# Kernel tuning notes

Measured on AMD Instinct MI355X. Metric: run time of the kernel, lower is better.

Reference implementation:

```python
import jax, jax.numpy as jnp
import numpy as np

D = 1024      # input_size / d_model
H = 16        # num_heads
HD = D // H   # head_size = 64
T = 2048      # block_size / seq_len
B = 2
FF = 4 * D
EPS = 1e-5


def setup_inputs() -> dict:
    key = jax.random.key(0)
    ks = jax.random.split(key, 16)
    s_in = 1.0 / np.sqrt(D)
    s_ff = 1.0 / np.sqrt(FF)
    return {
        "x": jax.random.normal(ks[0], (B, T, D), dtype=jnp.float32),
        # per-head unbiased projections, stacked over heads: [H, D, HD]
        "wq": jax.random.normal(ks[1], (H, D, HD), dtype=jnp.float32) * s_in,
        "wk": jax.random.normal(ks[2], (H, D, HD), dtype=jnp.float32) * s_in,
        "wv": jax.random.normal(ks[3], (H, D, HD), dtype=jnp.float32) * s_in,
        "w_proj": jax.random.normal(ks[4], (D, D), dtype=jnp.float32) * s_in,
        "b_proj": jnp.zeros((D,), dtype=jnp.float32),
        "ln1_g": jnp.ones((D,), dtype=jnp.float32),
        "ln1_b": jnp.zeros((D,), dtype=jnp.float32),
        "ln2_g": jnp.ones((D,), dtype=jnp.float32),
        "ln2_b": jnp.zeros((D,), dtype=jnp.float32),
        "w1": jax.random.normal(ks[5], (D, FF), dtype=jnp.float32) * s_in,
        "b1": jnp.zeros((FF,), dtype=jnp.float32),
        "w2": jax.random.normal(ks[6], (FF, D), dtype=jnp.float32) * s_ff,
        "b2": jnp.zeros((D,), dtype=jnp.float32),
    }


def _layernorm(x, g, b):
    mu = jnp.mean(x, axis=-1, keepdims=True)
    var = jnp.mean(jnp.square(x - mu), axis=-1, keepdims=True)
    return (x - mu) * jax.lax.rsqrt(var + EPS) * g + b


def reference(x, wq, wk, wv, w_proj, b_proj, ln1_g, ln1_b, ln2_g, ln2_b, w1, b1, w2, b2):
    Bv, Tv, _ = x.shape
    h = _layernorm(x, ln1_g, ln1_b)                       # [B,T,D]
    q = jnp.einsum("btc,hcd->bhtd", h, wq)
    k = jnp.einsum("btc,hcd->bhtd", h, wk)
    v = jnp.einsum("btc,hcd->bhtd", h, wv)
    scores = jnp.einsum("bhtd,bhsd->bhts", q, k) * (HD ** -0.5)  # [B,H,T,T]
    causal = jnp.tril(jnp.ones((Tv, Tv), dtype=bool))
    scores = jnp.where(causal, scores, -jnp.inf)
    attn = jax.nn.softmax(scores, axis=-1)
    out = jnp.einsum("bhts,bhsd->bhtd", attn, v)          # [B,H,T,HD]
    out = out.transpose(0, 2, 1, 3).reshape(Bv, Tv, H * HD)  # concat heads
    out = out @ w_proj + b_proj
    x = x + out
    h2 = _layernorm(x, ln2_g, ln2_b)
    ff = jax.nn.gelu(h2 @ w1 + b1, approximate=False) @ w2 + b2
    return x + ff
```

## Files before the change

### kernel.cpp

```cpp
#include <hip/hip_runtime.h>
#include <hip/hip_bf16.h>
#include <cstdint>
#include <cstddef>
#include <math.h>

#define D_ 1024
#define H_ 16
#define HD_ 64
#define T_ 2048
#define B_ 2
#define FF_ 4096
#define BT_ (B_*T_)
#define NT_ 32

typedef unsigned short u16;
typedef __attribute__((ext_vector_type(8))) __bf16 bf16x8;
typedef __attribute__((ext_vector_type(8))) u16 u16x8;
typedef __attribute__((ext_vector_type(4))) float f32x4;

__device__ __forceinline__ u16 f2bf(float f) {
  unsigned u = __builtin_bit_cast(unsigned, f);
  u += 0x7FFFu + ((u >> 16) & 1u);
  return (u16)(u >> 16);
}

__device__ __forceinline__ unsigned cvt_pk_bf16(float a, float b) {
  unsigned r;
  asm("v_cvt_pk_bf16_f32 %0, %1, %2" : "=v"(r) : "v"(a), "v"(b));
  return r;
}

__device__ __forceinline__ void gload16(const void* g, void* l) {
  __builtin_amdgcn_global_load_lds((__attribute__((address_space(1))) void*)g,
                                   (__attribute__((address_space(3))) void*)l, 16, 0, 0);
}

__global__ __launch_bounds__(256) void transpose_all(
    const float* __restrict__ wq, const float* __restrict__ wk,
    const float* __restrict__ wv, const float* __restrict__ w_proj,
    const float* __restrict__ w1, const float* __restrict__ w2,
    u16* __restrict__ wqkv_t, u16* __restrict__ wproj_t,
    u16* __restrict__ w1t, u16* __restrict__ w2t) {
  __shared__ float tile[32][33];
  const int bid = blockIdx.x;
  const float* in; u16* out; int R, C, tx, ty;
  if (bid < 3072) {
    const int w = bid >> 10, rem = bid & 1023;
    const int z = rem >> 6, t = rem & 63;
    tx = t & 1; ty = t >> 1;
    R = D_; C = HD_;
    in  = (w == 0 ? wq : w == 1 ? wk : wv) + (size_t)z * R * C;
    out = wqkv_t + (size_t)w * D_ * D_ + (size_t)z * C * R;
  } else if (bid < 4096) {
    const int t = bid - 3072;
    tx = t & 31; ty = t >> 5;
    R = D_; C = D_; in = w_proj; out = wproj_t;
  } else if (bid < 8192) {
    const int t = bid - 4096;
    tx = t & 127; ty = t >> 7;
    R = D_; C = FF_; in = w1; out = w1t;
  } else {
    const int t = bid - 8192;
    tx = t & 31; ty = t >> 5;
    R = FF_; C = D_; in = w2; out = w2t;
  }
  const int x = tx * 32 + threadIdx.x;
  const int y0 = ty * 32 + threadIdx.y;
  #pragma unroll
  for (int j = 0; j < 32; j += 8)
    tile[threadIdx.y + j][threadIdx.x] = in[(size_t)(y0 + j) * C + x];
  __syncthreads();
  const int orr = ty * 32 + threadIdx.x;
  const int oc0 = tx * 32 + threadIdx.y;
  #pragma unroll
  for (int j = 0; j < 32; j += 8)
    out[(size_t)(oc0 + j) * R + orr] = f2bf(tile[threadIdx.x][threadIdx.y + j]);
}

__global__ __launch_bounds__(256) void ln_rows(const float* __restrict__ x,
    const float* __restrict__ g, const float* __restrict__ bb, u16* __restrict__ out) {
  const int row = blockIdx.x, tid = threadIdx.x;
  const float4 v = ((const float4*)(x + (size_t)row * D_))[tid];
  float s = v.x + v.y + v.z + v.w;
  float sq = v.x*v.x + v.y*v.y + v.z*v.z + v.w*v.w;
  #pragma unroll
  for (int m = 1; m < 64; m <<= 1) { s += __shfl_xor(s, m); sq += __shfl_xor(sq, m); }
  __shared__ float ss[4], qs[4];
  if ((tid & 63) == 0) { ss[tid >> 6] = s; qs[tid >> 6] = sq; }
  __syncthreads();
  s  = ss[0] + ss[1] + ss[2] + ss[3];
  sq = qs[0] + qs[1] + qs[2] + qs[3];
  const float mean = s * (1.f / D_);
  const float var  = sq * (1.f / D_) - mean * mean;
  const float rstd = rsqrtf(var + 1e-5f);
  const float4 gv = ((const float4*)g)[tid];
  const float4 bv = ((const float4*)bb)[tid];
  u16 o[4];
  o[0] = f2bf((v.x - mean) * rstd * gv.x + bv.x);
  o[1] = f2bf((v.y - mean) * rstd * gv.y + bv.y);
  o[2] = f2bf((v.z - mean) * rstd * gv.z + bv.z);
  o[3] = f2bf((v.w - mean) * rstd * gv.w + bv.w);
  *(ushort4*)(out + (size_t)row * D_ + tid * 4) = *(ushort4*)o;
}

template<int ACT, int BIAS, int OUTBF, int PARTIAL>
__global__ __launch_bounds__(256, 4) void gemm128(
    const u16* __restrict__ A, const u16* __restrict__ Bt,
    const float* __restrict__ bias, const float* resid,
    void* Cout, int M, int N, int K, int Kper) {
  __shared__ __attribute__((aligned(16))) u16 LA[2][128 * 32];
  __shared__ __attribute__((aligned(16))) u16 LB[2][128 * 32];

  const int tid = threadIdx.x;
  const int wid = tid >> 6, lane = tid & 63;
  const int wr = wid >> 1, wc = wid & 1;
  const int frow = lane & 15, hi = lane >> 4;

  const int gx = gridDim.x;
  const int nwg = gx * gridDim.y;
  const int orig = blockIdx.y * gx + blockIdx.x;
  const int cpx = nwg >> 3;
  const int swz = (orig & 7) * cpx + (orig >> 3);
  const int bm = (swz / gx) * 128, bn = (swz % gx) * 128;
  const int z = PARTIAL ? blockIdx.z : 0;
  const int koff = z * Kper;
  const int nt = Kper >> 5;

  const int srow = tid >> 2;
  const int gch  = (tid & 3) ^ (srow & 3);
  const u16* Ag0 = A + (size_t)(bm + srow) * K + koff + gch * 8;
  const u16* Ag1 = Ag0 + (size_t)64 * K;
  const u16* Bg0 = Bt + (size_t)(bn + srow) * K + koff + gch * 8;
  const u16* Bg1 = Bg0 + (size_t)64 * K;
  const int ldsA0 = (wid * 16) * 32, ldsA1 = (64 + wid * 16) * 32;

  f32x4 acc[4][4] = {};

  #define STAGE32(kt, db)                              \
    {                                                  \
      const int ko = (kt) * 32;                        \
      gload16(Ag0 + ko, &LA[db][ldsA0]);               \
      gload16(Ag1 + ko, &LA[db][ldsA1]);               \
      gload16(Bg0 + ko, &LB[db][ldsA0]);               \
      gload16(Bg1 + ko, &LB[db][ldsA1]);               \
    }

  STAGE32(0, 0);

  for (int t = 0; t < nt; ++t) {
    const int db = t & 1;
    if (t + 1 < nt) {
      STAGE32(t + 1, db ^ 1);
      asm volatile("s_waitcnt vmcnt(4)" ::: "memory");
    } else {
      asm volatile("s_waitcnt vmcnt(0)" ::: "memory");
    }
    __builtin_amdgcn_s_barrier();

    const u16* Ab = &LA[db][0];
    const u16* Bb = &LB[db][0];

    bf16x8 af[4], bfr[4];
    #pragma unroll
    for (int i = 0; i < 4; i++) {
      const int ra = wr * 64 + i * 16 + frow;
      af[i]  = *(const bf16x8*)(Ab + ra * 32 + ((hi ^ (ra & 3)) << 3));
      const int rb = wc * 64 + i * 16 + frow;
      bfr[i] = *(const bf16x8*)(Bb + rb * 32 + ((hi ^ (rb & 3)) << 3));
    }
    __builtin_amdgcn_s_setprio(1);
    #pragma unroll
    for (int mi = 0; mi < 4; mi++)
      #pragma unroll
      for (int ni = 0; ni < 4; ni++)
        acc[mi][ni] = __builtin_amdgcn_mfma_f32_16x16x32_bf16(af[mi], bfr[ni], acc[mi][ni], 0, 0, 0);
    __builtin_amdgcn_s_setprio(0);
    __builtin_amdgcn_s_barrier();
  }
  #undef STAGE32

  const int r0 = bm + wr * 64 + hi * 4;
  const int c0 = bn + wc * 64 + frow;
  #pragma unroll
  for (int mi = 0; mi < 4; mi++) {
    #pragma unroll
    for (int ni = 0; ni < 4; ni++) {
      #pragma unroll
      for (int r = 0; r < 4; r++) {
        float v = acc[mi][ni][r];
        const int rr = r0 + mi * 16 + r;
        const int cc = c0 + ni * 16;
        if (PARTIAL) {
          ((float*)Cout)[((size_t)z * M + rr) * N + cc] = v;
        } else {
          if (BIAS) v += bias[cc];
          if (ACT == 1) {
            const float u = v * (0.79788456f + 0.03567740814f * v * v);
            const float e = exp2f(fminf(u * 2.885390082f, 80.f));
            v = v - v * __builtin_amdgcn_rcpf(1.0f + e);
          }
          if (resid) v += resid[(size_t)rr * N + cc];
          if (OUTBF) ((u16*)Cout)[(size_t)rr * N + cc] = f2bf(v);
          else       ((float*)Cout)[(size_t)rr * N + cc] = v;
        }
      }
    }
  }
}

template<int NPART>
__global__ __launch_bounds__(256) void reduce_parts(
    const float* __restrict__ parts, const float* __restrict__ bias,
    const float* __restrict__ resid, float* __restrict__ out, int MN, int N) {
  const int i4 = (blockIdx.x * 256 + threadIdx.x) * 4;
  if (i4 >= MN) return;
  float4 s = *(const float4*)(parts + i4);
  #pragma unroll
  for (int p = 1; p < NPART; p++) {
    const float4 t = *(const float4*)(parts + (size_t)p * MN + i4);
    s.x += t.x; s.y += t.y; s.z += t.z; s.w += t.w;
  }
  const float4 bv = *(const float4*)(bias + (i4 & (N - 1)));
  const float4 rv = *(const float4*)(resid + i4);
  s.x += bv.x + rv.x; s.y += bv.y + rv.y; s.z += bv.z + rv.z; s.w += bv.w + rv.w;
  *(float4*)(out + i4) = s;
}

__global__ __launch_bounds__(256) void reduce2_ln(
    const float* __restrict__ parts, const float* __restrict__ bias,
    const float* __restrict__ resid, const float* __restrict__ g,
    const float* __restrict__ bb, float* __restrict__ xout,
    u16* __restrict__ h2, int MN) {
  const int row = blockIdx.x, tid = threadIdx.x;
  const int i4 = row * D_ + tid * 4;
  float4 s = *(const float4*)(parts + i4);
  const float4 t = *(const float4*)(parts + (size_t)MN + i4);
  const float4 bv = *(const float4*)(bias + tid * 4);
  const float4 rv = *(const float4*)(resid + i4);
  s.x += t.x + bv.x + rv.x; s.y += t.y + bv.y + rv.y;
  s.z += t.z + bv.z + rv.z; s.w += t.w + bv.w + rv.w;
  *(float4*)(xout + i4) = s;
  float sm = s.x + s.y + s.z + s.w;
  float sq = s.x*s.x + s.y*s.y + s.z*s.z + s.w*s.w;
  #pragma unroll
  for (int m = 1; m < 64; m <<= 1) { sm += __shfl_xor(sm, m); sq += __shfl_xor(sq, m); }
  __shared__ float ss[4], qs[4];
  if ((tid & 63) == 0) { ss[tid >> 6] = sm; qs[tid >> 6] = sq; }
  __syncthreads();
  sm = ss[0] + ss[1] + ss[2] + ss[3];
  sq = qs[0] + qs[1] + qs[2] + qs[3];
  const float mean = sm * (1.f / D_);
  const float var  = sq * (1.f / D_) - mean * mean;
  const float rstd = rsqrtf(var + 1e-5f);
  const float4 gv = ((const float4*)g)[tid];
  const float4 b2v = ((const float4*)bb)[tid];
  u16 o[4];
  o[0] = f2bf((s.x - mean) * rstd * gv.x + b2v.x);
  o[1] = f2bf((s.y - mean) * rstd * gv.y + b2v.y);
  o[2] = f2bf((s.z - mean) * rstd * gv.z + b2v.z);
  o[3] = f2bf((s.w - mean) * rstd * gv.w + b2v.w);
  *(ushort4*)(h2 + (size_t)row * D_ + tid * 4) = *(ushort4*)o;
}

__global__ __launch_bounds__(256) void repack_qkv(const u16* __restrict__ qkv,
    u16* __restrict__ q, u16* __restrict__ k, u16* __restrict__ vt) {
  const int t0 = blockIdx.x * 64, bh = blockIdx.y;
  const int b = bh >> 4, h = bh & 15;
  const int tid = threadIdx.x;
  const int c = (tid & 7) * 8;
  __shared__ __attribute__((aligned(16))) u16 vs[64][72];
  #pragma unroll
  for (int p = 0; p < 2; p++) {
    const int tl = p * 32 + (tid >> 3);
    const size_t inrow = ((size_t)b * T_ + t0 + tl) * 3072 + h * 64;
    u16x8 qv = *(const u16x8*)(qkv + inrow + c);
    bf16x8 kv = *(const bf16x8*)(qkv + inrow + 1024 + c);
    bf16x8 vv = *(const bf16x8*)(qkv + inrow + 2048 + c);
    alignas(16) u16 qs[8];
    #pragma unroll
    for (int e = 0; e < 8; e++) {
      const float f = __builtin_bit_cast(float, ((unsigned)qv[e]) << 16) * 0.18033688011112042f;
      qs[e] = f2bf(f);
    }
    *(u16x8*)(q + ((size_t)bh * T_ + t0 + tl) * HD_ + c) = *(u16x8*)qs;
    *(bf16x8*)(k + ((size_t)bh * T_ + t0 + tl) * HD_ + c) = kv;
    *(bf16x8*)&vs[tl][c] = vv;
  }
  __syncthreads();
  const int d = tid >> 2, tc = (tid & 3) * 16;
  alignas(16) u16 tmp[16];
  #pragma unroll
  for (int j = 0; j < 16; j++) tmp[j] = vs[tc + j][d];
  *(bf16x8*)(vt + ((size_t)bh * HD_ + d) * T_ + t0 + tc)     = *(bf16x8*)&tmp[0];
  *(bf16x8*)(vt + ((size_t)bh * HD_ + d) * T_ + t0 + tc + 8) = *(bf16x8*)&tmp[8];
}

__global__ __launch_bounds__(512) void attn_fwd(
    const u16* __restrict__ q, const u16* __restrict__ k,
    const u16* __restrict__ vt, u16* __restrict__ out) {
  __shared__ __attribute__((aligned(16))) u16 Ps[8][16 * 64];
  __shared__ __attribute__((aligned(16))) u16 Kb[2][64 * 64];
  __shared__ __attribute__((aligned(16))) u16 Vb[2][64 * 64];

  const int bid = blockIdx.x;
  const int xcd = bid & 7, j = bid >> 3;
  const int bh  = xcd + 8 * (j & 3);
  const int qb  = 15 - (j >> 2);
  const int b = bh >> 4, h = bh & 15;
  const int tid = threadIdx.x, wid = tid >> 6, lane = tid & 63;
  const u16* kh = k  + (size_t)bh * T_ * HD_;
  const u16* vh = vt + (size_t)bh * HD_ * T_;
  const int q0 = qb * 128;
  const int nkt = 2 * qb + 2;
  const int wlast = 2 * qb + (wid >> 2);

  const int frow = lane & 15;
  const int hi   = lane >> 4;
  const int fk   = hi * 8;
  const int rowb = hi * 4;
  const int colb = frow;
  const int srow = tid >> 3;
  const int gch  = (tid & 7) ^ (srow & 7);

  u16x8 onebits = (u16x8)((u16)0x3F80);
  bf16x8 b_one = (frow == 0) ? __builtin_bit_cast(bf16x8, onebits) : (bf16x8){};

  u16* Pw = &Ps[wid][0];

  const u16* qrow = q + ((size_t)bh * T_ + q0 + wid * 16 + frow) * HD_;
  bf16x8 aq[2];
  aq[0] = *(const bf16x8*)(qrow + fk);
  aq[1] = *(const bf16x8*)(qrow + 32 + fk);

  float m2[4] = {-3e38f, -3e38f, -3e38f, -3e38f};
  f32x4 acc_l = {};
  f32x4 acc_o[4] = {};

  int cur = 0;
  gload16(kh + (size_t)srow * HD_ + gch * 8, &Kb[0][(wid * 8) * 64]);
  gload16(vh + (size_t)srow * T_ + gch * 8,  &Vb[0][(wid * 8) * 64]);
  __syncthreads();

  for (int kt = 0; kt < nkt; ++kt) {
    if (kt + 1 < nkt) {
      const int nx = cur ^ 1, ktn = kt + 1;
      gload16(kh + (size_t)(ktn * 64 + srow) * HD_ + gch * 8, &Kb[nx][(wid * 8) * 64]);
      gload16(vh + (size_t)srow * T_ + ktn * 64 + gch * 8,    &Vb[nx][(wid * 8) * 64]);
    }

    if (kt <= wlast) {
      const u16* Kc = &Kb[cur][0];
      const u16* Vc = &Vb[cur][0];

      float p2[4][4];
      __builtin_amdgcn_s_setprio(1);
      #pragma unroll
      for (int ni = 0; ni < 4; ni++) {
        f32x4 s = {};
        #pragma unroll
        for (int ks = 0; ks < 2; ks++) {
          const int row = ni * 16 + frow;
          const int ch  = ks * 4 + hi;
          bf16x8 bk = *(const bf16x8*)(Kc + row * 64 + ((ch ^ (row & 7)) << 3));
          s = __builtin_amdgcn_mfma_f32_16x16x32_bf16(aq[ks], bk, s, 0, 0, 0);
        }
        #pragma unroll
        for (int r = 0; r < 4; r++) p2[ni][r] = s[r];
      }
      __builtin_amdgcn_s_setprio(0);

      if (kt >= nkt - 2) {
        #pragma unroll
        for (int ni = 0; ni < 4; ni++)
          #pragma unroll
          for (int r = 0; r < 4; r++) {
            const bool msk = (kt * 64 + ni * 16 + colb) > (q0 + wid * 16 + rowb + r);
            if (msk) p2[ni][r] = -3e38f;
          }
      }

      float lmax[4];
      #pragma unroll
      for (int r = 0; r < 4; r++)
        lmax[r] = fmaxf(fmaxf(p2[0][r], p2[1][r]), fmaxf(p2[2][r], p2[3][r]));
      int ok = 1;
      #pragma unroll
      for (int r = 0; r < 4; r++) ok &= (lmax[r] <= m2[r] + 8.0f);
      if (!__all(ok)) {
        #pragma unroll
        for (int r = 0; r < 4; r++) {
          float rm = lmax[r];
          rm = fmaxf(rm, __shfl_xor(rm, 1));
          rm = fmaxf(rm, __shfl_xor(rm, 2));
          rm = fmaxf(rm, __shfl_xor(rm, 4));
          rm = fmaxf(rm, __shfl_xor(rm, 8));
          const float mnew = fmaxf(m2[r], rm);
          const float corr = exp2f(m2[r] - mnew);
          m2[r] = mnew;
          acc_l[r] *= corr;
          #pragma unroll
          for (int ni = 0; ni < 4; ni++) acc_o[ni][r] *= corr;
        }
      }
      #pragma unroll
      for (int ni = 0; ni < 4; ni++)
        #pragma unroll
        for (int r = 0; r < 4; r++) p2[ni][r] = exp2f(p2[ni][r] - m2[r]);

      #pragma unroll
      for (int ni = 0; ni < 4; ni++) {
        #pragma unroll
        for (int r = 0; r < 4; r += 2) {
          const unsigned pk = cvt_pk_bf16(p2[ni][r], p2[ni][r + 1]);
          const int lr0 = rowb + r, lr1 = rowb + r + 1;
          const int ch = ni * 2 + (colb >> 3);
          Pw[lr0 * 64 + ((ch ^ (lr0 & 7)) << 3) + (colb & 7)] = (u16)pk;
          Pw[lr1 * 64 + ((ch ^ (lr1 & 7)) << 3) + (colb & 7)] = (u16)(pk >> 16);
        }
      }
      bf16x8 ap[2];
      {
        const int c0 = (0 * 4 + hi) ^ (frow & 7);
        const int c1 = (1 * 4 + hi) ^ (frow & 7);
        ap[0] = *(const bf16x8*)(Pw + frow * 64 + (c0 << 3));
        ap[1] = *(const bf16x8*)(Pw + frow * 64 + (c1 << 3));
      }

      __builtin_amdgcn_s_setprio(1);
      #pragma unroll
      for (int ks = 0; ks < 2; ks++)
        acc_l = __builtin_amdgcn_mfma_f32_16x16x32_bf16(ap[ks], b_one, acc_l, 0, 0, 0);
      #pragma unroll
      for (int ni = 0; ni < 4; ni++) {
        #pragma unroll
        for (int ks = 0; ks < 2; ks++) {
          const int row = ni * 16 + frow;
          const int ch  = ks * 4 + hi;
          bf16x8 bv = *(const bf16x8*)(Vc + row * 64 + ((ch ^ (row & 7)) << 3));
          acc_o[ni] = __builtin_amdgcn_mfma_f32_16x16x32_bf16(ap[ks], bv, acc_o[ni], 0, 0, 0);
        }
      }
      __builtin_amdgcn_s_setprio(0);
    }

    __syncthreads();
    cur ^= 1;
  }

  float linv[4];
  #pragma unroll
  for (int r = 0; r < 4; r++) {
    const float lv = __shfl(acc_l[r], lane & 48);
    linv[r] = 1.0f / lv;
  }
  #pragma unroll
  for (int ni = 0; ni < 4; ni++)
    #pragma unroll
    for (int r = 0; r < 4; r++) {
      const float ov = acc_o[ni][r] * linv[r];
      const size_t row = (size_t)b * T_ + q0 + wid * 16 + rowb + r;
      out[row * D_ + h * HD_ + ni * 16 + colb] = f2bf(ov);
    }
}

extern "C" void kernel_launch(void* const* d_in, const int* in_sizes, int n_in,
                              void* d_out, int out_size, void* d_ws, size_t ws_size,
                              hipStream_t stream) {
  (void)in_sizes; (void)n_in; (void)out_size; (void)ws_size;
  const float* x      = (const float*)d_in[0];
  const float* wq     = (const float*)d_in[1];
  const float* wk     = (const float*)d_in[2];
  const float* wv     = (const float*)d_in[3];
  const float* w_proj = (const float*)d_in[4];
  const float* b_proj = (const float*)d_in[5];
  const float* ln1_g  = (const float*)d_in[6];
  const float* ln1_b  = (const float*)d_in[7];
  const float* ln2_g  = (const float*)d_in[8];
  const float* ln2_b  = (const float*)d_in[9];
  const float* w1     = (const float*)d_in[10];
  const float* b1     = (const float*)d_in[11];
  const float* w2     = (const float*)d_in[12];
  const float* b2     = (const float*)d_in[13];

  uint8_t* ws = (uint8_t*)d_ws;
  const size_t MB = 1024 * 1024;
  u16* wqkv_t = (u16*)(ws + 0);
  u16* wproj_t = (u16*)(ws + 6 * MB);
  u16* w1t  = (u16*)(ws + 8 * MB);
  u16* w2t  = (u16*)(ws + 16 * MB);
  u16* hbuf = (u16*)(ws + 24 * MB);
  u16* qkv  = (u16*)(ws + 32 * MB);
  u16* qb   = (u16*)(ws + 56 * MB);
  u16* kb   = (u16*)(ws + 64 * MB);
  u16* vtb  = (u16*)(ws + 72 * MB);
  u16* aout = (u16*)(ws + 80 * MB);
  u16* h2   = (u16*)(ws + 88 * MB);
  u16* ff1  = (u16*)(ws + 96 * MB);
  float* pparts = (float*)(ws + 32 * MB);
  float* fparts = (float*)(ws + 32 * MB);
  float* xout = (float*)d_out;

  transpose_all<<<12288, dim3(32, 8), 0, stream>>>(
      wq, wk, wv, w_proj, w1, w2, wqkv_t, wproj_t, w1t, w2t);

  ln_rows<<<BT_, 256, 0, stream>>>(x, ln1_g, ln1_b, hbuf);

  gemm128<0,0,1,0><<<dim3(3072/128, BT_/128), 256, 0, stream>>>(
      hbuf, wqkv_t, nullptr, nullptr, qkv, BT_, 3072, D_, D_);

  repack_qkv<<<dim3(T_/64, B_*H_), 256, 0, stream>>>(qkv, qb, kb, vtb);

  attn_fwd<<<dim3(512), 512, 0, stream>>>(qb, kb, vtb, aout);

  gemm128<0,0,0,1><<<dim3(D_/128, BT_/128, 2), 256, 0, stream>>>(
      aout, wproj_t, nullptr, nullptr, pparts, BT_, D_, D_, D_/2);
  reduce2_ln<<<BT_, 256, 0, stream>>>(
      pparts, b_proj, x, ln2_g, ln2_b, xout, h2, BT_*D_);

  gemm128<1,1,1,0><<<dim3(FF_/128, BT_/128), 256, 0, stream>>>(
      h2, w1t, b1, nullptr, ff1, BT_, FF_, D_, D_);

  gemm128<0,0,0,1><<<dim3(D_/128, BT_/128, 4), 256, 0, stream>>>(
      ff1, w2t, nullptr, nullptr, fparts, BT_, D_, FF_, FF_/4);
  reduce_parts<4><<<(BT_*D_)/1024, 256, 0, stream>>>(
      fparts, b2, xout, xout, BT_*D_, D_);
}
```

Before: 249.2 us.

## Fuse QKV repack into GEMM epilogue and pair causal query blocks in attention

The QKV GEMM epilogue now writes Q (pre-scaled), K, and transposed V directly into per-head layouts, which removes the separate repack kernel and the round trip through the intermediate qkv buffer. The V-transpose store is scattered, with a stride of T elements per lane, so the epilogue stores may coalesce poorly. Separately, each attention workgroup now processes two query blocks (qp and 15-qp) in sequence with a 256-block grid. This balances the causal work per block so every block does the same amount, at the cost of fewer concurrent workgroups.

```diff
diff --git a/kernel.cpp b/kernel.cpp
--- a/kernel.cpp
+++ b/kernel.cpp
@@ -103,7 +103,7 @@
   *(ushort4*)(out + (size_t)row * D_ + tid * 4) = *(ushort4*)o;
 }
 
-template<int ACT, int BIAS, int OUTBF, int PARTIAL>
+template<int ACT, int BIAS, int OUTBF, int PARTIAL, int QKVE>
 __global__ __launch_bounds__(256, 4) void gemm128(
     const u16* __restrict__ A, const u16* __restrict__ Bt,
     const float* __restrict__ bias, const float* resid,
@@ -190,7 +190,22 @@
         float v = acc[mi][ni][r];
         const int rr = r0 + mi * 16 + r;
         const int cc = c0 + ni * 16;
-        if (PARTIAL) {
+        if (QKVE) {
+          const int region = bn >> 10;
+          u16* qo = (u16*)Cout;
+          u16* ko = qo + (size_t)4 * 1024 * 1024;
+          u16* vo = qo + (size_t)8 * 1024 * 1024;
+          const int c1 = cc & 1023;
+          const int h = c1 >> 6, d = c1 & 63;
+          const int bb2 = rr >> 11, t2 = rr & 2047;
+          const int bh = bb2 * 16 + h;
+          if (region == 0)
+            qo[((size_t)bh * T_ + t2) * HD_ + d] = f2bf(v * 0.18033688011112042f);
+          else if (region == 1)
+            ko[((size_t)bh * T_ + t2) * HD_ + d] = f2bf(v);
+          else
+            vo[((size_t)bh * HD_ + d) * T_ + t2] = f2bf(v);
+        } else if (PARTIAL) {
           ((float*)Cout)[((size_t)z * M + rr) * N + cc] = v;
         } else {
           if (BIAS) v += bias[cc];
@@ -262,39 +277,6 @@
   *(ushort4*)(h2 + (size_t)row * D_ + tid * 4) = *(ushort4*)o;
 }
 
-__global__ __launch_bounds__(256) void repack_qkv(const u16* __restrict__ qkv,
-    u16* __restrict__ q, u16* __restrict__ k, u16* __restrict__ vt) {
-  const int t0 = blockIdx.x * 64, bh = blockIdx.y;
-  const int b = bh >> 4, h = bh & 15;
-  const int tid = threadIdx.x;
-  const int c = (tid & 7) * 8;
-  __shared__ __attribute__((aligned(16))) u16 vs[64][72];
-  #pragma unroll
-  for (int p = 0; p < 2; p++) {
-    const int tl = p * 32 + (tid >> 3);
-    const size_t inrow = ((size_t)b * T_ + t0 + tl) * 3072 + h * 64;
-    u16x8 qv = *(const u16x8*)(qkv + inrow + c);
-    bf16x8 kv = *(const bf16x8*)(qkv + inrow + 1024 + c);
-    bf16x8 vv = *(const bf16x8*)(qkv + inrow + 2048 + c);
-    alignas(16) u16 qs[8];
-    #pragma unroll
-    for (int e = 0; e < 8; e++) {
-      const float f = __builtin_bit_cast(float, ((unsigned)qv[e]) << 16) * 0.18033688011112042f;
-      qs[e] = f2bf(f);
-    }
-    *(u16x8*)(q + ((size_t)bh * T_ + t0 + tl) * HD_ + c) = *(u16x8*)qs;
-    *(bf16x8*)(k + ((size_t)bh * T_ + t0 + tl) * HD_ + c) = kv;
-    *(bf16x8*)&vs[tl][c] = vv;
-  }
-  __syncthreads();
-  const int d = tid >> 2, tc = (tid & 3) * 16;
-  alignas(16) u16 tmp[16];
-  #pragma unroll
-  for (int j = 0; j < 16; j++) tmp[j] = vs[tc + j][d];
-  *(bf16x8*)(vt + ((size_t)bh * HD_ + d) * T_ + t0 + tc)     = *(bf16x8*)&tmp[0];
-  *(bf16x8*)(vt + ((size_t)bh * HD_ + d) * T_ + t0 + tc + 8) = *(bf16x8*)&tmp[8];
-}
-
 __global__ __launch_bounds__(512) void attn_fwd(
     const u16* __restrict__ q, const u16* __restrict__ k,
     const u16* __restrict__ vt, u16* __restrict__ out) {
@@ -305,14 +287,11 @@
   const int bid = blockIdx.x;
   const int xcd = bid & 7, j = bid >> 3;
   const int bh  = xcd + 8 * (j & 3);
-  const int qb  = 15 - (j >> 2);
+  const int qp  = j >> 2;
   const int b = bh >> 4, h = bh & 15;
   const int tid = threadIdx.x, wid = tid >> 6, lane = tid & 63;
   const u16* kh = k  + (size_t)bh * T_ * HD_;
   const u16* vh = vt + (size_t)bh * HD_ * T_;
-  const int q0 = qb * 128;
-  const int nkt = 2 * qb + 2;
-  const int wlast = 2 * qb + (wid >> 2);
 
   const int frow = lane & 15;
   const int hi   = lane >> 4;
@@ -327,140 +306,147 @@
 
   u16* Pw = &Ps[wid][0];
 
-  const u16* qrow = q + ((size_t)bh * T_ + q0 + wid * 16 + frow) * HD_;
-  bf16x8 aq[2];
-  aq[0] = *(const bf16x8*)(qrow + fk);
-  aq[1] = *(const bf16x8*)(qrow + 32 + fk);
-
-  float m2[4] = {-3e38f, -3e38f, -3e38f, -3e38f};
-  f32x4 acc_l = {};
-  f32x4 acc_o[4] = {};
-
-  int cur = 0;
-  gload16(kh + (size_t)srow * HD_ + gch * 8, &Kb[0][(wid * 8) * 64]);
-  gload16(vh + (size_t)srow * T_ + gch * 8,  &Vb[0][(wid * 8) * 64]);
-  __syncthreads();
-
-  for (int kt = 0; kt < nkt; ++kt) {
-    if (kt + 1 < nkt) {
-      const int nx = cur ^ 1, ktn = kt + 1;
-      gload16(kh + (size_t)(ktn * 64 + srow) * HD_ + gch * 8, &Kb[nx][(wid * 8) * 64]);
-      gload16(vh + (size_t)srow * T_ + ktn * 64 + gch * 8,    &Vb[nx][(wid * 8) * 64]);
+  for (int qi = 0; qi < 2; ++qi) {
+    const int qb = qi ? (15 - qp) : qp;
+    const int q0 = qb * 128;
+    const int nkt = 2 * qb + 2;
+    const int wlast = 2 * qb + (wid >> 2);
+
+    const u16* qrow = q + ((size_t)bh * T_ + q0 + wid * 16 + frow) * HD_;
+    bf16x8 aq[2];
+    aq[0] = *(const bf16x8*)(qrow + fk);
+    aq[1] = *(const bf16x8*)(qrow + 32 + fk);
+
+    float m2[4] = {-3e38f, -3e38f, -3e38f, -3e38f};
+    f32x4 acc_l = {};
+    f32x4 acc_o[4] = {};
+
+    int cur = 0;
+    gload16(kh + (size_t)srow * HD_ + gch * 8, &Kb[0][(wid * 8) * 64]);
+    gload16(vh + (size_t)srow * T_ + gch * 8,  &Vb[0][(wid * 8) * 64]);
+    __syncthreads();
+
+    for (int kt = 0; kt < nkt; ++kt) {
+      if (kt + 1 < nkt) {
+        const int nx = cur ^ 1, ktn = kt + 1;
+        gload16(kh + (size_t)(ktn * 64 + srow) * HD_ + gch * 8, &Kb[nx][(wid * 8) * 64]);
+        gload16(vh + (size_t)srow * T_ + ktn * 64 + gch * 8,    &Vb[nx][(wid * 8) * 64]);
+      }
+
+      if (kt <= wlast) {
+        const u16* Kc = &Kb[cur][0];
+        const u16* Vc = &Vb[cur][0];
+
+        float p2[4][4];
+        __builtin_amdgcn_s_setprio(1);
+        #pragma unroll
+        for (int ni = 0; ni < 4; ni++) {
+          f32x4 s = {};
+          #pragma unroll
+          for (int ks = 0; ks < 2; ks++) {
+            const int row = ni * 16 + frow;
+            const int ch  = ks * 4 + hi;
+            bf16x8 bk = *(const bf16x8*)(Kc + row * 64 + ((ch ^ (row & 7)) << 3));
+            s = __builtin_amdgcn_mfma_f32_16x16x32_bf16(aq[ks], bk, s, 0, 0, 0);
+          }
+          #pragma unroll
+          for (int r = 0; r < 4; r++) p2[ni][r] = s[r];
+        }
+        __builtin_amdgcn_s_setprio(0);
+
+        if (kt >= nkt - 2) {
+          #pragma unroll
+          for (int ni = 0; ni < 4; ni++)
+            #pragma unroll
+            for (int r = 0; r < 4; r++) {
+              const bool msk = (kt * 64 + ni * 16 + colb) > (q0 + wid * 16 + rowb + r);
+              if (msk) p2[ni][r] = -3e38f;
+            }
+        }
+
+        float lmax[4];
+        #pragma unroll
+        for (int r = 0; r < 4; r++)
+          lmax[r] = fmaxf(fmaxf(p2[0][r], p2[1][r]), fmaxf(p2[2][r], p2[3][r]));
+        int ok = 1;
+        #pragma unroll
+        for (int r = 0; r < 4; r++) ok &= (lmax[r] <= m2[r] + 8.0f);
+        if (!__all(ok)) {
+          #pragma unroll
+          for (int r = 0; r < 4; r++) {
+            float rm = lmax[r];
+            rm = fmaxf(rm, __shfl_xor(rm, 1));
+            rm = fmaxf(rm, __shfl_xor(rm, 2));
+            rm = fmaxf(rm, __shfl_xor(rm, 4));
+            rm = fmaxf(rm, __shfl_xor(rm, 8));
+            const float mnew = fmaxf(m2[r], rm);
+            const float corr = exp2f(m2[r] - mnew);
+            m2[r] = mnew;
+            acc_l[r] *= corr;
+            #pragma unroll
+            for (int ni = 0; ni < 4; ni++) acc_o[ni][r] *= corr;
+          }
+        }
+        #pragma unroll
+        for (int ni = 0; ni < 4; ni++)
+          #pragma unroll
+          for (int r = 0; r < 4; r++) p2[ni][r] = exp2f(p2[ni][r] - m2[r]);
+
+        #pragma unroll
+        for (int ni = 0; ni < 4; ni++) {
+          #pragma unroll
+          for (int r = 0; r < 4; r += 2) {
+            const unsigned pk = cvt_pk_bf16(p2[ni][r], p2[ni][r + 1]);
+            const int lr0 = rowb + r, lr1 = rowb + r + 1;
+            const int ch = ni * 2 + (colb >> 3);
+            Pw[lr0 * 64 + ((ch ^ (lr0 & 7)) << 3) + (colb & 7)] = (u16)pk;
+            Pw[lr1 * 64 + ((ch ^ (lr1 & 7)) << 3) + (colb & 7)] = (u16)(pk >> 16);
+          }
+        }
+        bf16x8 ap[2];
+        {
+          const int c0 = (0 * 4 + hi) ^ (frow & 7);
+          const int c1 = (1 * 4 + hi) ^ (frow & 7);
+          ap[0] = *(const bf16x8*)(Pw + frow * 64 + (c0 << 3));
+          ap[1] = *(const bf16x8*)(Pw + frow * 64 + (c1 << 3));
+        }
+
+        __builtin_amdgcn_s_setprio(1);
+        #pragma unroll
+        for (int ks = 0; ks < 2; ks++)
+          acc_l = __builtin_amdgcn_mfma_f32_16x16x32_bf16(ap[ks], b_one, acc_l, 0, 0, 0);
+        #pragma unroll
+        for (int ni = 0; ni < 4; ni++) {
+          #pragma unroll
+          for (int ks = 0; ks < 2; ks++) {
+            const int row = ni * 16 + frow;
+            const int ch  = ks * 4 + hi;
+            bf16x8 bv = *(const bf16x8*)(Vc + row * 64 + ((ch ^ (row & 7)) << 3));
+            acc_o[ni] = __builtin_amdgcn_mfma_f32_16x16x32_bf16(ap[ks], bv, acc_o[ni], 0, 0, 0);
+          }
+        }
+        __builtin_amdgcn_s_setprio(0);
+      }
+
+      __syncthreads();
+      cur ^= 1;
     }
 
-    if (kt <= wlast) {
-      const u16* Kc = &Kb[cur][0];
-      const u16* Vc = &Vb[cur][0];
-
-      float p2[4][4];
-      __builtin_amdgcn_s_setprio(1);
-      #pragma unroll
-      for (int ni = 0; ni < 4; ni++) {
-        f32x4 s = {};
-        #pragma unroll
-        for (int ks = 0; ks < 2; ks++) {
-          const int row = ni * 16 + frow;
-          const int ch  = ks * 4 + hi;
-          bf16x8 bk = *(const bf16x8*)(Kc + row * 64 + ((ch ^ (row & 7)) << 3));
-          s = __builtin_amdgcn_mfma_f32_16x16x32_bf16(aq[ks], bk, s, 0, 0, 0);
-        }
-        #pragma unroll
-        for (int r = 0; r < 4; r++) p2[ni][r] = s[r];
-      }
-      __builtin_amdgcn_s_setprio(0);
-
-      if (kt >= nkt - 2) {
-        #pragma unroll
-        for (int ni = 0; ni < 4; ni++)
-          #pragma unroll
-          for (int r = 0; r < 4; r++) {
-            const bool msk = (kt * 64 + ni * 16 + colb) > (q0 + wid * 16 + rowb + r);
-            if (msk) p2[ni][r] = -3e38f;
-          }
-      }
-
-      float lmax[4];
-      #pragma unroll
-      for (int r = 0; r < 4; r++)
-        lmax[r] = fmaxf(fmaxf(p2[0][r], p2[1][r]), fmaxf(p2[2][r], p2[3][r]));
-      int ok = 1;
-      #pragma unroll
-      for (int r = 0; r < 4; r++) ok &= (lmax[r] <= m2[r] + 8.0f);
-      if (!__all(ok)) {
-        #pragma unroll
-        for (int r = 0; r < 4; r++) {
-          float rm = lmax[r];
-          rm = fmaxf(rm, __shfl_xor(rm, 1));
-          rm = fmaxf(rm, __shfl_xor(rm, 2));
-          rm = fmaxf(rm, __shfl_xor(rm, 4));
-          rm = fmaxf(rm, __shfl_xor(rm, 8));
-          const float mnew = fmaxf(m2[r], rm);
-          const float corr = exp2f(m2[r] - mnew);
-          m2[r] = mnew;
-          acc_l[r] *= corr;
-          #pragma unroll
-          for (int ni = 0; ni < 4; ni++) acc_o[ni][r] *= corr;
-        }
-      }
-      #pragma unroll
-      for (int ni = 0; ni < 4; ni++)
-        #pragma unroll
-        for (int r = 0; r < 4; r++) p2[ni][r] = exp2f(p2[ni][r] - m2[r]);
-
-      #pragma unroll
-      for (int ni = 0; ni < 4; ni++) {
-        #pragma unroll
-        for (int r = 0; r < 4; r += 2) {
-          const unsigned pk = cvt_pk_bf16(p2[ni][r], p2[ni][r + 1]);
-          const int lr0 = rowb + r, lr1 = rowb + r + 1;
-          const int ch = ni * 2 + (colb >> 3);
-          Pw[lr0 * 64 + ((ch ^ (lr0 & 7)) << 3) + (colb & 7)] = (u16)pk;
-          Pw[lr1 * 64 + ((ch ^ (lr1 & 7)) << 3) + (colb & 7)] = (u16)(pk >> 16);
-        }
-      }
-      bf16x8 ap[2];
-      {
-        const int c0 = (0 * 4 + hi) ^ (frow & 7);
-        const int c1 = (1 * 4 + hi) ^ (frow & 7);
-        ap[0] = *(const bf16x8*)(Pw + frow * 64 + (c0 << 3));
-        ap[1] = *(const bf16x8*)(Pw + frow * 64 + (c1 << 3));
-      }
-
-      __builtin_amdgcn_s_setprio(1);
-      #pragma unroll
-      for (int ks = 0; ks < 2; ks++)
-        acc_l = __builtin_amdgcn_mfma_f32_16x16x32_bf16(ap[ks], b_one, acc_l, 0, 0, 0);
-      #pragma unroll
-      for (int ni = 0; ni < 4; ni++) {
-        #pragma unroll
-        for (int ks = 0; ks < 2; ks++) {
-          const int row = ni * 16 + frow;
-          const int ch  = ks * 4 + hi;
-          bf16x8 bv = *(const bf16x8*)(Vc + row * 64 + ((ch ^ (row & 7)) << 3));
-          acc_o[ni] = __builtin_amdgcn_mfma_f32_16x16x32_bf16(ap[ks], bv, acc_o[ni], 0, 0, 0);
-        }
-      }
-      __builtin_amdgcn_s_setprio(0);
-    }
-
-    __syncthreads();
-    cur ^= 1;
-  }
-
-  float linv[4];
-  #pragma unroll
-  for (int r = 0; r < 4; r++) {
-    const float lv = __shfl(acc_l[r], lane & 48);
-    linv[r] = 1.0f / lv;
-  }
-  #pragma unroll
-  for (int ni = 0; ni < 4; ni++)
+    float linv[4];
     #pragma unroll
     for (int r = 0; r < 4; r++) {
-      const float ov = acc_o[ni][r] * linv[r];
-      const size_t row = (size_t)b * T_ + q0 + wid * 16 + rowb + r;
-      out[row * D_ + h * HD_ + ni * 16 + colb] = f2bf(ov);
+      const float lv = __shfl(acc_l[r], lane & 48);
+      linv[r] = 1.0f / lv;
     }
+    #pragma unroll
+    for (int ni = 0; ni < 4; ni++)
+      #pragma unroll
+      for (int r = 0; r < 4; r++) {
+        const float ov = acc_o[ni][r] * linv[r];
+        const size_t row = (size_t)b * T_ + q0 + wid * 16 + rowb + r;
+        out[row * D_ + h * HD_ + ni * 16 + colb] = f2bf(ov);
+      }
+  }
 }
 
 extern "C" void kernel_launch(void* const* d_in, const int* in_sizes, int n_in,
@@ -489,7 +475,6 @@
   u16* w1t  = (u16*)(ws + 8 * MB);
   u16* w2t  = (u16*)(ws + 16 * MB);
   u16* hbuf = (u16*)(ws + 24 * MB);
-  u16* qkv  = (u16*)(ws + 32 * MB);
   u16* qb   = (u16*)(ws + 56 * MB);
   u16* kb   = (u16*)(ws + 64 * MB);
   u16* vtb  = (u16*)(ws + 72 * MB);
@@ -505,22 +490,20 @@
 
   ln_rows<<<BT_, 256, 0, stream>>>(x, ln1_g, ln1_b, hbuf);
 
-  gemm128<0,0,1,0><<<dim3(3072/128, BT_/128), 256, 0, stream>>>(
-      hbuf, wqkv_t, nullptr, nullptr, qkv, BT_, 3072, D_, D_);
-
-  repack_qkv<<<dim3(T_/64, B_*H_), 256, 0, stream>>>(qkv, qb, kb, vtb);
-
-  attn_fwd<<<dim3(512), 512, 0, stream>>>(qb, kb, vtb, aout);
-
-  gemm128<0,0,0,1><<<dim3(D_/128, BT_/128, 2), 256, 0, stream>>>(
+  gemm128<0,0,0,0,1><<<dim3(3072/128, BT_/128), 256, 0, stream>>>(
+      hbuf, wqkv_t, nullptr, nullptr, qb, BT_, 3072, D_, D_);
+
+  attn_fwd<<<dim3(256), 512, 0, stream>>>(qb, kb, vtb, aout);
+
+  gemm128<0,0,0,1,0><<<dim3(D_/128, BT_/128, 2), 256, 0, stream>>>(
       aout, wproj_t, nullptr, nullptr, pparts, BT_, D_, D_, D_/2);
   reduce2_ln<<<BT_, 256, 0, stream>>>(
       pparts, b_proj, x, ln2_g, ln2_b, xout, h2, BT_*D_);
 
-  gemm128<1,1,1,0><<<dim3(FF_/128, BT_/128), 256, 0, stream>>>(
+  gemm128<1,1,1,0,0><<<dim3(FF_/128, BT_/128), 256, 0, stream>>>(
       h2, w1t, b1, nullptr, ff1, BT_, FF_, D_, D_);
 
-  gemm128<0,0,0,1><<<dim3(D_/128, BT_/128, 4), 256, 0, stream>>>(
+  gemm128<0,0,0,1,0><<<dim3(D_/128, BT_/128, 4), 256, 0, stream>>>(
       ff1, w2t, nullptr, nullptr, fparts, BT_, D_, FF_, FF_/4);
   reduce_parts<4><<<(BT_*D_)/1024, 256, 0, stream>>>(
       fparts, b2, xout, xout, BT_*D_, D_);
```

New measurement: 248.3 us. No clear change (-0.3%).
